# Optimization experiments

Measured on AMD Instinct MI355X. Metric: run time of the kernel, lower is better.

The kernel has to match this reference:

```python
import jax, jax.numpy as jnp
import numpy as np

NUM_HEADS = 8
ROPE_MIN_LOG = -12.0
ROPE_MAX_LOG = 0.0
EPS = 1e-6


def rms_norm(h, w):
    # per-head-dim RMSNorm in fp32 (Qwen3 style), no shift applied in forward
    dt = h.dtype
    h32 = h.astype(jnp.float32)
    var = jnp.mean(h32 * h32, axis=-1, keepdims=True)
    return (w * (h32 * jax.lax.rsqrt(var + EPS))).astype(dt)


def setup_inputs() -> dict:
    key = jax.random.key(0)
    k1, k2, k3 = jax.random.split(key, 3)
    B, H, W, C = 1, 256, 256, 512
    x = jax.random.normal(k1, (B, H, W, C), dtype=jnp.float32)
    w_qkv = jax.random.normal(k2, (3 * C, C), dtype=jnp.float32) * 0.02
    hd = C // NUM_HEADS
    q_norm_w = jnp.ones((hd,), dtype=jnp.float32)
    k_norm_w = jnp.ones((hd,), dtype=jnp.float32)
    w_proj = jax.random.normal(k3, (C, C), dtype=jnp.float32) * 0.02
    b_proj = jnp.zeros((C,), dtype=jnp.float32)
    return {"x": x, "w_qkv": w_qkv, "q_norm_w": q_norm_w, "k_norm_w": k_norm_w,
            "w_proj": w_proj, "b_proj": b_proj}


def reference(x, w_qkv, q_norm_w, k_norm_w, w_proj, b_proj):
    B, H, W, C = x.shape
    nh = NUM_HEADS
    hd = C // nh
    rope_dim = (hd // 2) * 2
    half = rope_dim // 2
    scale = hd ** -0.5

    # [B,H,W,C] -> [B*W, H, C]
    xr = jnp.transpose(x, (0, 2, 1, 3)).reshape(B * W, H, C)
    qkv = jnp.einsum('bhc,dc->bhd', xr, w_qkv)                # [BW, H, 3C]
    qkv = qkv.reshape(B * W, H, 3, nh, hd)
    qkv = jnp.transpose(qkv, (2, 0, 3, 1, 4))                 # [3, BW, nh, H, hd]
    q, k, v = qkv[0], qkv[1], qkv[2]

    q = rms_norm(q, q_norm_w)
    k = rms_norm(k, k_norm_w)

    # segmented-exponential RoPE along trace axis H (default normalized pos)
    pos = jnp.linspace(0.0, 1.0, H, dtype=jnp.float32)        # [H]
    freqs = jnp.exp(jnp.linspace(ROPE_MIN_LOG, ROPE_MAX_LOG, half, dtype=jnp.float32))
    ang = pos[:, None] * freqs[None, :] * jnp.float32(H)      # [H, half]
    cos = jnp.cos(ang)
    sin = jnp.sin(ang)

    def rope(t):
        rot = t[..., :rope_dim].reshape(B * W, nh, H, half, 2)
        te, to = rot[..., 0], rot[..., 1]
        e2 = te * cos - to * sin
        o2 = te * sin + to * cos
        rot2 = jnp.stack([e2, o2], axis=-1).reshape(B * W, nh, H, rope_dim)
        return jnp.concatenate([rot2, t[..., rope_dim:]], axis=-1)

    q = rope(q)
    k = rope(k)

    # SDPA (non-causal, no dropout)
    scores = jnp.einsum('bnqd,bnkd->bnqk', q, k) * scale      # [BW, nh, H, H]
    attn = jax.nn.softmax(scores, axis=-1)
    o = jnp.einsum('bnqk,bnkd->bnqd', attn, v)                # [BW, nh, H, hd]

    o = jnp.transpose(o, (0, 2, 1, 3)).reshape(B * W, H, C)
    out = jnp.einsum('bhc,dc->bhd', o, w_proj) + b_proj
    out = out.reshape(B, W, H, C)
    return jnp.transpose(out, (0, 2, 1, 3))                   # [B, H, W, C]
```

## Files before the change

### kernel.cpp

```cpp
#include <hip/hip_runtime.h>
#include <hip/hip_bf16.h>
#include <cstdint>
#include <cstddef>

#define SEQ 256
#define WDIM 256
#define CDIM 512
#define NHEAD 8
#define HD 64
#define NTOK (SEQ*WDIM)
#define NTT 8

typedef __attribute__((ext_vector_type(8))) short bf16x8;
typedef __attribute__((ext_vector_type(4))) float f32x4;

static __device__ __forceinline__ unsigned short f2bf(float f) {
  __hip_bfloat16 h = __float2bfloat16(f);
  return *reinterpret_cast<unsigned short*>(&h);
}

__global__ void k_convert(const float* __restrict__ x,
                          const float* __restrict__ wqkv,
                          const float* __restrict__ wproj,
                          unsigned short* __restrict__ xb,
                          unsigned short* __restrict__ wqb,
                          unsigned short* __restrict__ wpb) {
  const int NX = NTOK*CDIM/4, NQ = 3*CDIM*CDIM/4, NP = CDIM*CDIM/4;
  const int total = NX + NQ + NP;
  for (int i = blockIdx.x*blockDim.x + threadIdx.x; i < total; i += gridDim.x*blockDim.x) {
    const float4* s; unsigned short* d; int j;
    if (i < NX)           { s = (const float4*)x;     d = xb;  j = i; }
    else if (i < NX+NQ)   { s = (const float4*)wqkv;  d = wqb; j = i-NX; }
    else                  { s = (const float4*)wproj; d = wpb; j = i-NX-NQ; }
    float4 f = s[j];
    ushort4 o;
    o.x = f2bf(f.x); o.y = f2bf(f.y); o.z = f2bf(f.z); o.w = f2bf(f.w);
    ((ushort4*)d)[j] = o;
  }
}

__global__ void k_rope(float2* __restrict__ tab) {
  int i = blockIdx.x*blockDim.x + threadIdx.x;
  if (i >= SEQ*32) return;
  int h = i >> 5, j = i & 31;
  float freq = expf(-12.0f + 12.0f*(float)j/31.0f);
  float ang = ((float)h/255.0f) * freq * 256.0f;
  tab[i] = make_float2(cosf(ang), sinf(ang));
}


#define STAGE_G(tau_, part_)                                                              \
  if ((tau_) < NTT) {                                                                     \
    const int buf_ = (tau_) & 1;                                                          \
    const int ab_ = (part_) >> 1, hh_ = (part_) & 1;                                      \
    const unsigned short* src_ = ab_ ? B : A;                                             \
    const int row0_ = (ab_ ? rowB0 : rowA0) + hh_*128;                                    \
    _Pragma("unroll")                                                                     \
    for (int c_ = 0; c_ < 2; ++c_) {                                                      \
      int G_ = wid*128 + c_*64 + lane;                                                    \
      int r_ = G_ >> 3, g_ = G_ & 7;                                                      \
      int gsw_ = g_ ^ (r_ & 7);                                                           \
      __builtin_amdgcn_global_load_lds(                                                   \
        (const __attribute__((address_space(1))) unsigned int*)                           \
          ((const char*)src_ + (size_t)(row0_ + r_)*1024 + (size_t)(tau_)*128 + gsw_*16), \
        (__attribute__((address_space(3))) unsigned int*)                                 \
          ((char*)&L[buf_][ab_][hh_][0] + G_*16),                                         \
        16, 0, 0);                                                                        \
    }                                                                                     \
  }

#define LDA_(dst, m_, kk_)                                                                 \
  { int r_ = (m_)*16 + li;                                                                 \
    dst = *(const bf16x8*)((const char*)&L[buf][0][wr][0] + r_*128 + (((((kk_)*4)+lg) ^ (r_ & 7))<<4)); }
#define LDB_(dst, n_, kk_)                                                                 \
  { int r_ = (wc & 1)*64 + (n_)*16 + li;                                                   \
    dst = *(const bf16x8*)((const char*)&L[buf][1][wc>>1][0] + r_*128 + (((((kk_)*4)+lg) ^ (r_ & 7))<<4)); }

#define PH_SYNC                                            \
  __builtin_amdgcn_s_barrier();                            \
  asm volatile("s_waitcnt lgkmcnt(0)" ::: "memory");       \
  __builtin_amdgcn_sched_barrier(0);

#define MFMA16(afr, bfr, mo)                                                               \
  __builtin_amdgcn_s_setprio(1);                                                          \
  _Pragma("unroll")                                                                        \
  for (int m = 0; m < 4; ++m)                                                              \
    _Pragma("unroll")                                                                      \
    for (int n = 0; n < 4; ++n)                                                            \
      acc[m+(mo)][n] = __builtin_amdgcn_mfma_f32_16x16x32_bf16(afr[m], bfr[n], acc[m+(mo)][n], 0, 0, 0); \
  __builtin_amdgcn_s_setprio(0);

__device__ __forceinline__ void gemm256(const unsigned short* __restrict__ A,
                                        const unsigned short* __restrict__ B,
                                        int rowA0, int rowB0,
                                        unsigned short (&L)[2][2][2][128*64],
                                        f32x4 (&acc)[8][4]) {
  const int tid = threadIdx.x;
  const int lane = tid & 63, wid = tid >> 6;
  const int wr = wid >> 2, wc = wid & 3;
  const int li = lane & 15, lg = lane >> 4;

  STAGE_G(0,0) STAGE_G(0,1) STAGE_G(0,2) STAGE_G(0,3) STAGE_G(1,0) STAGE_G(1,1)
  asm volatile("s_waitcnt vmcnt(4)" ::: "memory");
  __builtin_amdgcn_s_barrier();

  #pragma unroll 1
  for (int tau = 0; tau < NTT; ++tau) {
    const int buf = tau & 1;
    bf16x8 a0[4], a1[4], aL0[4], aL1[4], bb0[4], bb1[4];
    #pragma unroll
    for (int m = 0; m < 4; ++m) LDA_(a0[m], m, 0);
    #pragma unroll
    for (int n = 0; n < 4; ++n) LDB_(bb0[n], n, 0);
    STAGE_G(tau+1, 2)
    PH_SYNC
    MFMA16(a0, bb0, 0)
    __builtin_amdgcn_s_barrier();
    #pragma unroll
    for (int m = 0; m < 4; ++m) LDA_(a1[m], m+4, 0);
    #pragma unroll
    for (int m = 0; m < 4; ++m) LDA_(aL0[m], m, 1);
    STAGE_G(tau+1, 3)
    PH_SYNC
    MFMA16(a1, bb0, 4)
    __builtin_amdgcn_s_barrier();
    #pragma unroll
    for (int m = 0; m < 4; ++m) LDA_(aL1[m], m+4, 1);
    #pragma unroll
    for (int n = 0; n < 4; ++n) LDB_(bb1[n], n, 1);
    PH_SYNC
    MFMA16(aL0, bb1, 0)
    __builtin_amdgcn_s_barrier();
    STAGE_G(tau+2, 0)
    STAGE_G(tau+2, 1)
    __builtin_amdgcn_sched_barrier(0);
    MFMA16(aL1, bb1, 4)
    if (tau < NTT-2) { asm volatile("s_waitcnt vmcnt(4)" ::: "memory"); }
    else             { asm volatile("s_waitcnt vmcnt(0)" ::: "memory"); }
    __builtin_amdgcn_s_barrier();
  }
}

__launch_bounds__(512)
__global__ void k_qkv(const unsigned short* __restrict__ A,
                      const unsigned short* __restrict__ B,
                      const float* __restrict__ qnw, const float* __restrict__ knw,
                      const float2* __restrict__ rope,
                      unsigned short* __restrict__ Qw,
                      unsigned short* __restrict__ Kw,
                      unsigned short* __restrict__ Vw) {
  __shared__ __align__(16) unsigned short L[2][2][2][128*64];
  int wg = (blockIdx.x & 7)*192 + (blockIdx.x >> 3);
  int bn = wg % 6, bm = wg / 6;
  f32x4 acc[8][4] = {};
  gemm256(A, B, bm*256, bn*256, L, acc);

  const int lane = threadIdx.x & 63, wid = threadIdx.x >> 6;
  const int wr = wid >> 2, wc = wid & 3;
  const int li = lane & 15, lg = lane >> 4;
  int d0 = bn*256 + wc*64;
  int third = d0 >> 9;
  int nhh = (d0 >> 6) & 7;
  int t0 = bm*256 + wr*128;
  int hpos = bm;

  if (third == 2) {
    #pragma unroll
    for (int m = 0; m < 8; ++m)
      #pragma unroll
      for (int n = 0; n < 4; ++n)
        #pragma unroll
        for (int r = 0; r < 4; ++r) {
          int t = t0 + m*16 + lg*4 + r;
          int wI = t & 255;
          int e = n*16 + li;
          Vw[((size_t)(wI*8 + nhh)*256 + hpos)*64 + e] = f2bf(acc[m][n][r]);
        }
  } else {
    const float* nw = (third == 0) ? qnw : knw;
    unsigned short* dst = (third == 0) ? Qw : Kw;
    const float qsc = (third == 0) ? 0.125f : 1.0f;
    float nwv[4]; float2 cs[4];
    #pragma unroll
    for (int n = 0; n < 4; ++n) {
      int e = n*16 + li;
      nwv[n] = nw[e];
      cs[n] = rope[hpos*32 + (e >> 1)];
    }
    bool odd = (li & 1) != 0;
    #pragma unroll
    for (int m = 0; m < 8; ++m) {
      float rsg[4];
      #pragma unroll
      for (int r = 0; r < 4; ++r) {
        float p = 0.f;
        #pragma unroll
        for (int n = 0; n < 4; ++n) p += acc[m][n][r]*acc[m][n][r];
        #pragma unroll
        for (int d = 1; d < 16; d <<= 1) p += __shfl_xor(p, d, 64);
        rsg[r] = rsqrtf(p*(1.0f/64.0f) + 1e-6f);
      }
      #pragma unroll
      for (int n = 0; n < 4; ++n)
        #pragma unroll
        for (int r = 0; r < 4; ++r) {
          float v = acc[m][n][r] * rsg[r] * nwv[n];
          float pr = __shfl_xor(v, 1, 64);
          float res = odd ? (pr*cs[n].y + v*cs[n].x) : (v*cs[n].x - pr*cs[n].y);
          res *= qsc;
          int t = t0 + m*16 + lg*4 + r;
          int wI = t & 255;
          int e = n*16 + li;
          dst[((size_t)(wI*8 + nhh)*256 + hpos)*64 + e] = f2bf(res);
        }
    }
  }
}

__launch_bounds__(256, 2)
__global__ void k_attn(const unsigned short* __restrict__ Q,
                       const unsigned short* __restrict__ K,
                       const unsigned short* __restrict__ V,
                       unsigned short* __restrict__ O) {
  __shared__ __align__(16) unsigned short P_lds[4][64*64];
  __shared__ __align__(16) unsigned short VT_lds[64*72];
  __shared__ __align__(16) unsigned short V_stage[64*64];
  int b = blockIdx.x;
  const unsigned short* Qb = Q + (size_t)b*SEQ*HD;
  const unsigned short* Kb = K + (size_t)b*SEQ*HD;
  const unsigned short* Vb = V + (size_t)b*SEQ*HD;
  const int lane = threadIdx.x & 63, wid = threadIdx.x >> 6;
  const int li = lane & 15, lg = lane >> 4;
  const int q0 = wid*64;
  char* Pw = (char*)&P_lds[wid][0];

#define STAGE_V(c_)                                                                       \
  { _Pragma("unroll")                                                                     \
    for (int r_ = 0; r_ < 2; ++r_) {                                                      \
      int D_ = wid*128 + r_*64 + lane;                                                    \
      int kl_ = D_ >> 3, g_ = (D_ & 7) ^ (kl_ & 7);                                       \
      __builtin_amdgcn_global_load_lds(                                                   \
        (const __attribute__((address_space(1))) unsigned int*)                           \
          (Vb + (size_t)((c_)*64 + kl_)*64 + g_*8),                                       \
        (__attribute__((address_space(3))) unsigned int*)((char*)V_stage + D_*16),        \
        16, 0, 0);                                                                        \
    } }

  STAGE_V(0)

  bf16x8 qf[4][2];
  #pragma unroll
  for (int n = 0; n < 4; ++n)
    #pragma unroll
    for (int kk = 0; kk < 2; ++kk)
      qf[n][kk] = *(const bf16x8*)(Qb + (q0 + n*16 + li)*64 + kk*32 + lg*8);

  f32x4 oa[4][4] = {};
  float mrun[4], lrun[4];
  #pragma unroll
  for (int n = 0; n < 4; ++n) { mrun[n] = -1e30f; lrun[n] = 0.0f; }

  #pragma unroll 1
  for (int kb = 0; kb < 4; ++kb) {
    int key0 = kb*64;
    f32x4 s[4][4] = {};
    #pragma unroll
    for (int kk = 0; kk < 2; ++kk) {
      bf16x8 kf[4];
      #pragma unroll
      for (int m = 0; m < 4; ++m)
        kf[m] = *(const bf16x8*)(Kb + (key0 + m*16 + li)*64 + kk*32 + lg*8);
      __builtin_amdgcn_s_setprio(1);
      #pragma unroll
      for (int m = 0; m < 4; ++m)
        #pragma unroll
        for (int n = 0; n < 4; ++n)
          s[m][n] = __builtin_amdgcn_mfma_f32_16x16x32_bf16(kf[m], qf[n][kk], s[m][n], 0, 0, 0);
      __builtin_amdgcn_s_setprio(0);
    }
    float mx[4], al[4];
    #pragma unroll
    for (int n = 0; n < 4; ++n) {
      float v = -1e30f;
      #pragma unroll
      for (int m = 0; m < 4; ++m)
        #pragma unroll
        for (int r = 0; r < 4; ++r) v = fmaxf(v, s[m][n][r]);
      v = fmaxf(v, __shfl_xor(v, 16, 64));
      v = fmaxf(v, __shfl_xor(v, 32, 64));
      float mn = fmaxf(mrun[n], v);
      al[n] = __expf(mrun[n] - mn);
      mrun[n] = mn;
      mx[n] = mn;
    }
    float rs[4] = {0.f,0.f,0.f,0.f};
    #pragma unroll
    for (int m = 0; m < 4; ++m)
      #pragma unroll
      for (int n = 0; n < 4; ++n) {
        f32x4 sv = s[m][n];
        #pragma unroll
        for (int r = 0; r < 4; ++r) {
          float p = __expf(sv[r] - mx[n]);
          sv[r] = p; rs[n] += p;
        }
        unsigned lo = (unsigned)f2bf(sv[0]) | ((unsigned)f2bf(sv[1]) << 16);
        unsigned hi = (unsigned)f2bf(sv[2]) | ((unsigned)f2bf(sv[3]) << 16);
        uint2 pk; pk.x = lo; pk.y = hi;
        int q = n*16 + li;
        int off = (q*128 + (m*16 + lg*4)*2) ^ ((li & 7) << 4);
        *(uint2*)(Pw + off) = pk;
      }
    #pragma unroll
    for (int n = 0; n < 4; ++n) {
      rs[n] += __shfl_xor(rs[n], 16, 64);
      rs[n] += __shfl_xor(rs[n], 32, 64);
      lrun[n] = lrun[n]*al[n] + rs[n];
    }
    #pragma unroll
    for (int mp = 0; mp < 4; ++mp)
      #pragma unroll
      for (int r = 0; r < 4; ++r) {
        float a = __shfl(al[mp], lg*4 + r, 64);
        #pragma unroll
        for (int np = 0; np < 4; ++np) oa[mp][np][r] *= a;
      }
    asm volatile("s_waitcnt vmcnt(0)" ::: "memory");
    __builtin_amdgcn_s_barrier();
    #pragma unroll
    for (int gi = 0; gi < 2; ++gi) {
      int g = wid + gi*4;
      bf16x8 row = *(const bf16x8*)&V_stage[(lane*8 + (g ^ (lane & 7)))*8];
      #pragma unroll
      for (int j = 0; j < 8; ++j)
        VT_lds[(g*8 + j)*72 + lane] = (unsigned short)row[j];
    }
    __builtin_amdgcn_s_barrier();
    if (kb < 3) STAGE_V(kb+1)
    #pragma unroll
    for (int kk = 0; kk < 2; ++kk) {
      bf16x8 pf[4], vf[4];
      #pragma unroll
      for (int mp = 0; mp < 4; ++mp) {
        int q = mp*16 + li;
        int off = (q*128 + (kk*32 + lg*8)*2) ^ ((li & 7) << 4);
        pf[mp] = *(const bf16x8*)(Pw + off);
      }
      #pragma unroll
      for (int np = 0; np < 4; ++np)
        vf[np] = *(const bf16x8*)&VT_lds[(np*16 + li)*72 + kk*32 + lg*8];
      __builtin_amdgcn_s_setprio(1);
      #pragma unroll
      for (int mp = 0; mp < 4; ++mp)
        #pragma unroll
        for (int np = 0; np < 4; ++np)
          oa[mp][np] = __builtin_amdgcn_mfma_f32_16x16x32_bf16(pf[mp], vf[np], oa[mp][np], 0, 0, 0);
      __builtin_amdgcn_s_setprio(0);
    }
  }
  int wseq = b >> 3, whead = b & 7;
  #pragma unroll
  for (int mp = 0; mp < 4; ++mp)
    #pragma unroll
    for (int r = 0; r < 4; ++r) {
      float linv = 1.0f / __shfl(lrun[mp], lg*4 + r, 64);
      #pragma unroll
      for (int np = 0; np < 4; ++np) {
        int q = q0 + mp*16 + lg*4 + r;
        int e = np*16 + li;
        O[((size_t)q*WDIM + wseq)*CDIM + whead*HD + e] = f2bf(oa[mp][np][r] * linv);
      }
    }
}

__launch_bounds__(512)
__global__ void k_proj(const unsigned short* __restrict__ A,
                       const unsigned short* __restrict__ B,
                       const float* __restrict__ bias,
                       float* __restrict__ out) {
  __shared__ __align__(16) unsigned short L[2][2][2][128*64];
  int wg = (blockIdx.x & 7)*64 + (blockIdx.x >> 3);
  int bn = wg & 1, bm = wg >> 1;
  f32x4 acc[8][4] = {};
  gemm256(A, B, bm*256, bn*256, L, acc);

  const int lane = threadIdx.x & 63, wid = threadIdx.x >> 6;
  const int wr = wid >> 2, wc = wid & 3;
  const int li = lane & 15, lg = lane >> 4;
  int d0 = bn*256 + wc*64;
  int t0 = bm*256 + wr*128;
  float bi[4];
  #pragma unroll
  for (int n = 0; n < 4; ++n) bi[n] = bias[d0 + n*16 + li];
  #pragma unroll
  for (int m = 0; m < 8; ++m)
    #pragma unroll
    for (int n = 0; n < 4; ++n)
      #pragma unroll
      for (int r = 0; r < 4; ++r)
        out[(size_t)(t0 + m*16 + lg*4 + r)*CDIM + d0 + n*16 + li] = acc[m][n][r] + bi[n];
}

extern "C" void kernel_launch(void* const* d_in, const int* in_sizes, int n_in,
                              void* d_out, int out_size, void* d_ws, size_t ws_size,
                              hipStream_t stream) {
  (void)in_sizes; (void)n_in; (void)out_size; (void)ws_size;
  const float* x     = (const float*)d_in[0];
  const float* wqkv  = (const float*)d_in[1];
  const float* qnw   = (const float*)d_in[2];
  const float* knw   = (const float*)d_in[3];
  const float* wproj = (const float*)d_in[4];
  const float* bproj = (const float*)d_in[5];
  float* out = (float*)d_out;
  char* ws = (char*)d_ws;

  const size_t SZ_X = (size_t)NTOK*CDIM*2;
  unsigned short* xb  = (unsigned short*)(ws);
  unsigned short* wqb = (unsigned short*)(ws + SZ_X);
  unsigned short* wpb = (unsigned short*)(ws + SZ_X + 1572864);
  float2*         rp  = (float2*)       (ws + SZ_X + 1572864 + 524288);
  unsigned short* Qw  = (unsigned short*)(ws + SZ_X + 1572864 + 524288 + 65536);
  unsigned short* Kw  = (unsigned short*)((char*)Qw + SZ_X);
  unsigned short* Vw  = (unsigned short*)((char*)Kw + SZ_X);
  unsigned short* Ow  = xb;

  k_convert<<<dim3(2048), dim3(256), 0, stream>>>(x, wqkv, wproj, xb, wqb, wpb);
  k_rope   <<<dim3(32),   dim3(256), 0, stream>>>(rp);
  k_qkv    <<<dim3(1536), dim3(512), 0, stream>>>(xb, wqb, qnw, knw, rp, Qw, Kw, Vw);
  k_attn   <<<dim3(2048), dim3(256), 0, stream>>>(Qw, Kw, Vw, Ow);
  k_proj   <<<dim3(512),  dim3(512), 0, stream>>>(Ow, wpb, bproj, out);
}
```

Baseline: 322.7 us.

## Fuse fp32-to-bf16 conversion of x into QKV GEMM A-operand loading

Drops the separate conversion pass over the 64K×512 activation tensor. The QKV GEMM now reads fp32 x straight into registers, converts it to bf16 and writes it into swizzled LDS, while B still uses direct global-to-LDS loads. This saves a full write and re-read of a 64 MB bf16 copy and one kernel launch. In exchange the GEMM reads fp32 A tiles at twice the byte volume, and each tile is re-read once per column block (six times). The register staging adds VGPR pressure and extra waitcnt/barrier points in the pipelined loop.

```diff
diff --git a/kernel.cpp b/kernel.cpp
--- a/kernel.cpp
+++ b/kernel.cpp
@@ -13,30 +13,24 @@
 
 typedef __attribute__((ext_vector_type(8))) short bf16x8;
 typedef __attribute__((ext_vector_type(4))) float f32x4;
+typedef __attribute__((ext_vector_type(8))) unsigned short u16x8;
 
 static __device__ __forceinline__ unsigned short f2bf(float f) {
   __hip_bfloat16 h = __float2bfloat16(f);
   return *reinterpret_cast<unsigned short*>(&h);
 }
 
-__global__ void k_convert(const float* __restrict__ x,
-                          const float* __restrict__ wqkv,
-                          const float* __restrict__ wproj,
-                          unsigned short* __restrict__ xb,
-                          unsigned short* __restrict__ wqb,
-                          unsigned short* __restrict__ wpb) {
-  const int NX = NTOK*CDIM/4, NQ = 3*CDIM*CDIM/4, NP = CDIM*CDIM/4;
-  const int total = NX + NQ + NP;
-  for (int i = blockIdx.x*blockDim.x + threadIdx.x; i < total; i += gridDim.x*blockDim.x) {
-    const float4* s; unsigned short* d; int j;
-    if (i < NX)           { s = (const float4*)x;     d = xb;  j = i; }
-    else if (i < NX+NQ)   { s = (const float4*)wqkv;  d = wqb; j = i-NX; }
-    else                  { s = (const float4*)wproj; d = wpb; j = i-NX-NQ; }
-    float4 f = s[j];
-    ushort4 o;
-    o.x = f2bf(f.x); o.y = f2bf(f.y); o.z = f2bf(f.z); o.w = f2bf(f.w);
-    ((ushort4*)d)[j] = o;
-  }
+__global__ void k_convw(const float* __restrict__ wqkv, const float* __restrict__ wproj,
+                        unsigned short* __restrict__ wqb, unsigned short* __restrict__ wpb) {
+  const int NQ = 3*CDIM*CDIM/4;
+  int i = blockIdx.x*blockDim.x + threadIdx.x;
+  const float4* s; unsigned short* d; int j;
+  if (i < NQ) { s = (const float4*)wqkv;  d = wqb; j = i; }
+  else        { s = (const float4*)wproj; d = wpb; j = i - NQ; }
+  float4 f = s[j];
+  ushort4 o;
+  o.x = f2bf(f.x); o.y = f2bf(f.y); o.z = f2bf(f.z); o.w = f2bf(f.w);
+  ((ushort4*)d)[j] = o;
 }
 
 __global__ void k_rope(float2* __restrict__ tab) {
@@ -48,6 +42,27 @@
   tab[i] = make_float2(cosf(ang), sinf(ang));
 }
 
+
+#define LDA_(dst, m_, kk_)                                                                 \
+  { int r_ = (m_)*16 + li;                                                                 \
+    dst = *(const bf16x8*)((const char*)&L[buf][0][wr][0] + r_*128 + (((((kk_)*4)+lg) ^ (r_ & 7))<<4)); }
+#define LDB_(dst, n_, kk_)                                                                 \
+  { int r_ = (wc & 1)*64 + (n_)*16 + li;                                                   \
+    dst = *(const bf16x8*)((const char*)&L[buf][1][wc>>1][0] + r_*128 + (((((kk_)*4)+lg) ^ (r_ & 7))<<4)); }
+
+#define PH_SYNC                                            \
+  __builtin_amdgcn_s_barrier();                            \
+  asm volatile("s_waitcnt lgkmcnt(0)" ::: "memory");       \
+  __builtin_amdgcn_sched_barrier(0);
+
+#define MFMA16(afr, bfr, mo)                                                               \
+  __builtin_amdgcn_s_setprio(1);                                                          \
+  _Pragma("unroll")                                                                        \
+  for (int m = 0; m < 4; ++m)                                                              \
+    _Pragma("unroll")                                                                      \
+    for (int n = 0; n < 4; ++n)                                                            \
+      acc[m+(mo)][n] = __builtin_amdgcn_mfma_f32_16x16x32_bf16(afr[m], bfr[n], acc[m+(mo)][n], 0, 0, 0); \
+  __builtin_amdgcn_s_setprio(0);
 
 #define STAGE_G(tau_, part_)                                                              \
   if ((tau_) < NTT) {                                                                     \
@@ -69,27 +84,6 @@
     }                                                                                     \
   }
 
-#define LDA_(dst, m_, kk_)                                                                 \
-  { int r_ = (m_)*16 + li;                                                                 \
-    dst = *(const bf16x8*)((const char*)&L[buf][0][wr][0] + r_*128 + (((((kk_)*4)+lg) ^ (r_ & 7))<<4)); }
-#define LDB_(dst, n_, kk_)                                                                 \
-  { int r_ = (wc & 1)*64 + (n_)*16 + li;                                                   \
-    dst = *(const bf16x8*)((const char*)&L[buf][1][wc>>1][0] + r_*128 + (((((kk_)*4)+lg) ^ (r_ & 7))<<4)); }
-
-#define PH_SYNC                                            \
-  __builtin_amdgcn_s_barrier();                            \
-  asm volatile("s_waitcnt lgkmcnt(0)" ::: "memory");       \
-  __builtin_amdgcn_sched_barrier(0);
-
-#define MFMA16(afr, bfr, mo)                                                               \
-  __builtin_amdgcn_s_setprio(1);                                                          \
-  _Pragma("unroll")                                                                        \
-  for (int m = 0; m < 4; ++m)                                                              \
-    _Pragma("unroll")                                                                      \
-    for (int n = 0; n < 4; ++n)                                                            \
-      acc[m+(mo)][n] = __builtin_amdgcn_mfma_f32_16x16x32_bf16(afr[m], bfr[n], acc[m+(mo)][n], 0, 0, 0); \
-  __builtin_amdgcn_s_setprio(0);
-
 __device__ __forceinline__ void gemm256(const unsigned short* __restrict__ A,
                                         const unsigned short* __restrict__ B,
                                         int rowA0, int rowB0,
@@ -141,8 +135,109 @@
   }
 }
 
+
+#define STAGE_B(tau_, hh_)                                                                \
+  if ((tau_) < NTT) {                                                                     \
+    const int buf_ = (tau_) & 1;                                                          \
+    _Pragma("unroll")                                                                     \
+    for (int c_ = 0; c_ < 2; ++c_) {                                                      \
+      int G_ = wid*128 + c_*64 + lane;                                                    \
+      int r_ = G_ >> 3, g_ = G_ & 7;                                                      \
+      int gsw_ = g_ ^ (r_ & 7);                                                           \
+      __builtin_amdgcn_global_load_lds(                                                   \
+        (const __attribute__((address_space(1))) unsigned int*)                           \
+          ((const char*)B + (size_t)(rowB0 + (hh_)*128 + r_)*1024 + (size_t)(tau_)*128 + gsw_*16), \
+        (__attribute__((address_space(3))) unsigned int*)                                 \
+          ((char*)&L[buf_][1][hh_][0] + G_*16),                                           \
+        16, 0, 0);                                                                        \
+    }                                                                                     \
+  }
+
+#define ALOAD_H(tau_, h_)                                                                 \
+  if ((tau_) < NTT) {                                                                     \
+    _Pragma("unroll")                                                                     \
+    for (int j_ = 0; j_ < 4; ++j_)                                                        \
+      areg[h_][j_] = *(const float4*)((const char*)A +                                    \
+        (size_t)(rowA0 + (h_)*128 + arow)*2048 + (size_t)(tau_)*256 + acb + j_*16);       \
+  }
+
+#define AWRITE_H(tau_, h_)                                                                \
+  if ((tau_) < NTT) {                                                                     \
+    const int buf_ = (tau_) & 1;                                                          \
+    _Pragma("unroll")                                                                     \
+    for (int gi_ = 0; gi_ < 2; ++gi_) {                                                   \
+      float4 f0 = areg[h_][gi_*2], f1 = areg[h_][gi_*2+1];                                \
+      u16x8 pk_;                                                                          \
+      pk_[0]=f2bf(f0.x); pk_[1]=f2bf(f0.y); pk_[2]=f2bf(f0.z); pk_[3]=f2bf(f0.w);         \
+      pk_[4]=f2bf(f1.x); pk_[5]=f2bf(f1.y); pk_[6]=f2bf(f1.z); pk_[7]=f2bf(f1.w);         \
+      int g_ = (acb >> 5) + gi_;                                                          \
+      *(u16x8*)((char*)&L[buf_][0][h_][0] + arow*128 + ((g_ ^ (arow & 7))<<4)) = pk_;     \
+    }                                                                                     \
+  }
+
+__device__ __forceinline__ void gemm256_f32(const float* __restrict__ A,
+                                            const unsigned short* __restrict__ B,
+                                            int rowA0, int rowB0,
+                                            unsigned short (&L)[2][2][2][128*64],
+                                            f32x4 (&acc)[8][4]) {
+  const int tid = threadIdx.x;
+  const int lane = tid & 63, wid = tid >> 6;
+  const int wr = wid >> 2, wc = wid & 3;
+  const int li = lane & 15, lg = lane >> 4;
+  const int arow = tid >> 2, acb = (tid & 3)*64;
+  float4 areg[2][4];
+
+  STAGE_B(0, 0) STAGE_B(0, 1)
+  ALOAD_H(0, 0) ALOAD_H(0, 1)
+  asm volatile("s_waitcnt vmcnt(0)" ::: "memory");
+  AWRITE_H(0, 0) AWRITE_H(0, 1)
+  asm volatile("s_waitcnt lgkmcnt(0)" ::: "memory");
+  __builtin_amdgcn_s_barrier();
+
+  #pragma unroll 1
+  for (int tau = 0; tau < NTT; ++tau) {
+    const int buf = tau & 1;
+    bf16x8 a0[4], a1[4], aL0[4], aL1[4], bb0[4], bb1[4];
+    #pragma unroll
+    for (int m = 0; m < 4; ++m) LDA_(a0[m], m, 0);
+    #pragma unroll
+    for (int n = 0; n < 4; ++n) LDB_(bb0[n], n, 0);
+    STAGE_B(tau+1, 0)
+    __builtin_amdgcn_sched_barrier(0);
+    ALOAD_H(tau+1, 0)
+    PH_SYNC
+    MFMA16(a0, bb0, 0)
+    __builtin_amdgcn_s_barrier();
+    #pragma unroll
+    for (int m = 0; m < 4; ++m) LDA_(a1[m], m+4, 0);
+    STAGE_B(tau+1, 1)
+    __builtin_amdgcn_sched_barrier(0);
+    ALOAD_H(tau+1, 1)
+    PH_SYNC
+    MFMA16(a1, bb0, 4)
+    __builtin_amdgcn_s_barrier();
+    #pragma unroll
+    for (int m = 0; m < 4; ++m) LDA_(aL0[m], m, 1);
+    #pragma unroll
+    for (int m = 0; m < 4; ++m) LDA_(aL1[m], m+4, 1);
+    #pragma unroll
+    for (int n = 0; n < 4; ++n) LDB_(bb1[n], n, 1);
+    asm volatile("s_waitcnt vmcnt(6)" ::: "memory");
+    AWRITE_H(tau+1, 0)
+    PH_SYNC
+    MFMA16(aL0, bb1, 0)
+    __builtin_amdgcn_s_barrier();
+    asm volatile("s_waitcnt vmcnt(0)" ::: "memory");
+    AWRITE_H(tau+1, 1)
+    __builtin_amdgcn_sched_barrier(0);
+    MFMA16(aL1, bb1, 4)
+    asm volatile("s_waitcnt lgkmcnt(0)" ::: "memory");
+    __builtin_amdgcn_s_barrier();
+  }
+}
+
 __launch_bounds__(512)
-__global__ void k_qkv(const unsigned short* __restrict__ A,
+__global__ void k_qkv(const float* __restrict__ A,
                       const unsigned short* __restrict__ B,
                       const float* __restrict__ qnw, const float* __restrict__ knw,
                       const float2* __restrict__ rope,
@@ -153,7 +248,7 @@
   int wg = (blockIdx.x & 7)*192 + (blockIdx.x >> 3);
   int bn = wg % 6, bm = wg / 6;
   f32x4 acc[8][4] = {};
-  gemm256(A, B, bm*256, bn*256, L, acc);
+  gemm256_f32(A, B, bm*256, bn*256, L, acc);
 
   const int lane = threadIdx.x & 63, wid = threadIdx.x >> 6;
   const int wr = wid >> 2, wc = wid & 3;
@@ -415,18 +510,17 @@
   char* ws = (char*)d_ws;
 
   const size_t SZ_X = (size_t)NTOK*CDIM*2;
-  unsigned short* xb  = (unsigned short*)(ws);
-  unsigned short* wqb = (unsigned short*)(ws + SZ_X);
-  unsigned short* wpb = (unsigned short*)(ws + SZ_X + 1572864);
-  float2*         rp  = (float2*)       (ws + SZ_X + 1572864 + 524288);
-  unsigned short* Qw  = (unsigned short*)(ws + SZ_X + 1572864 + 524288 + 65536);
+  unsigned short* wqb = (unsigned short*)(ws);
+  unsigned short* wpb = (unsigned short*)(ws + 1572864);
+  float2*         rp  = (float2*)       (ws + 1572864 + 524288);
+  unsigned short* Qw  = (unsigned short*)(ws + 1572864 + 524288 + 65536);
   unsigned short* Kw  = (unsigned short*)((char*)Qw + SZ_X);
   unsigned short* Vw  = (unsigned short*)((char*)Kw + SZ_X);
-  unsigned short* Ow  = xb;
-
-  k_convert<<<dim3(2048), dim3(256), 0, stream>>>(x, wqkv, wproj, xb, wqb, wpb);
+  unsigned short* Ow  = (unsigned short*)((char*)Vw + SZ_X);
+
+  k_convw  <<<dim3(1024), dim3(256), 0, stream>>>(wqkv, wproj, wqb, wpb);
   k_rope   <<<dim3(32),   dim3(256), 0, stream>>>(rp);
-  k_qkv    <<<dim3(1536), dim3(512), 0, stream>>>(xb, wqb, qnw, knw, rp, Qw, Kw, Vw);
+  k_qkv    <<<dim3(1536), dim3(512), 0, stream>>>(x, wqb, qnw, knw, rp, Qw, Kw, Vw);
   k_attn   <<<dim3(2048), dim3(256), 0, stream>>>(Qw, Kw, Vw, Ow);
   k_proj   <<<dim3(512),  dim3(512), 0, stream>>>(Ow, wpb, bproj, out);
 }
```

New measurement: 376.5 us. 1.17x slower.

## Prefetch V into registers and skip online-softmax rescale when max grows little

Applied to the files above, without the earlier changes.

V tiles are now prefetched straight into registers with plain global loads instead of async global-to-LDS staging, which removes the V_stage buffer and the vmcnt wait. Each wave also skips the running-max update and the rescaling of the output accumulator unless some row's max grows by more than 8, using a lazy-rescale threshold. This cuts exp and shuffle work and frees LDS, which may help occupancy. The cost is extra vector registers for vrow, and exponentials taken against a stale max can reach up to e^8, which still fits in fp32 and bf16.

```diff
diff --git a/kernel.cpp b/kernel.cpp
--- a/kernel.cpp
+++ b/kernel.cpp
@@ -224,7 +224,6 @@
                        unsigned short* __restrict__ O) {
   __shared__ __align__(16) unsigned short P_lds[4][64*64];
   __shared__ __align__(16) unsigned short VT_lds[64*72];
-  __shared__ __align__(16) unsigned short V_stage[64*64];
   int b = blockIdx.x;
   const unsigned short* Qb = Q + (size_t)b*SEQ*HD;
   const unsigned short* Kb = K + (size_t)b*SEQ*HD;
@@ -234,19 +233,10 @@
   const int q0 = wid*64;
   char* Pw = (char*)&P_lds[wid][0];
 
-#define STAGE_V(c_)                                                                       \
-  { _Pragma("unroll")                                                                     \
-    for (int r_ = 0; r_ < 2; ++r_) {                                                      \
-      int D_ = wid*128 + r_*64 + lane;                                                    \
-      int kl_ = D_ >> 3, g_ = (D_ & 7) ^ (kl_ & 7);                                       \
-      __builtin_amdgcn_global_load_lds(                                                   \
-        (const __attribute__((address_space(1))) unsigned int*)                           \
-          (Vb + (size_t)((c_)*64 + kl_)*64 + g_*8),                                       \
-        (__attribute__((address_space(3))) unsigned int*)((char*)V_stage + D_*16),        \
-        16, 0, 0);                                                                        \
-    } }
-
-  STAGE_V(0)
+  bf16x8 vrow[2];
+  #pragma unroll
+  for (int gi = 0; gi < 2; ++gi)
+    vrow[gi] = *(const bf16x8*)(Vb + (size_t)lane*64 + (wid + gi*4)*8);
 
   bf16x8 qf[4][2];
   #pragma unroll
@@ -278,7 +268,7 @@
           s[m][n] = __builtin_amdgcn_mfma_f32_16x16x32_bf16(kf[m], qf[n][kk], s[m][n], 0, 0, 0);
       __builtin_amdgcn_s_setprio(0);
     }
-    float mx[4], al[4];
+    float vmx[4];
     #pragma unroll
     for (int n = 0; n < 4; ++n) {
       float v = -1e30f;
@@ -288,10 +278,32 @@
         for (int r = 0; r < 4; ++r) v = fmaxf(v, s[m][n][r]);
       v = fmaxf(v, __shfl_xor(v, 16, 64));
       v = fmaxf(v, __shfl_xor(v, 32, 64));
-      float mn = fmaxf(mrun[n], v);
-      al[n] = __expf(mrun[n] - mn);
-      mrun[n] = mn;
-      mx[n] = mn;
+      vmx[n] = v;
+    }
+    float dmax = -1e30f;
+    #pragma unroll
+    for (int n = 0; n < 4; ++n) dmax = fmaxf(dmax, vmx[n] - mrun[n]);
+    float mx[4];
+    if (!__all(dmax <= 8.0f)) {
+      float al[4];
+      #pragma unroll
+      for (int n = 0; n < 4; ++n) {
+        float mn = fmaxf(mrun[n], vmx[n]);
+        al[n] = __expf(mrun[n] - mn);
+        mrun[n] = mn; mx[n] = mn;
+        lrun[n] *= al[n];
+      }
+      #pragma unroll
+      for (int mp = 0; mp < 4; ++mp)
+        #pragma unroll
+        for (int r = 0; r < 4; ++r) {
+          float a = __shfl(al[mp], lg*4 + r, 64);
+          #pragma unroll
+          for (int np = 0; np < 4; ++np) oa[mp][np][r] *= a;
+        }
+    } else {
+      #pragma unroll
+      for (int n = 0; n < 4; ++n) mx[n] = mrun[n];
     }
     float rs[4] = {0.f,0.f,0.f,0.f};
     #pragma unroll
@@ -315,28 +327,23 @@
     for (int n = 0; n < 4; ++n) {
       rs[n] += __shfl_xor(rs[n], 16, 64);
       rs[n] += __shfl_xor(rs[n], 32, 64);
-      lrun[n] = lrun[n]*al[n] + rs[n];
-    }
-    #pragma unroll
-    for (int mp = 0; mp < 4; ++mp)
-      #pragma unroll
-      for (int r = 0; r < 4; ++r) {
-        float a = __shfl(al[mp], lg*4 + r, 64);
-        #pragma unroll
-        for (int np = 0; np < 4; ++np) oa[mp][np][r] *= a;
-      }
-    asm volatile("s_waitcnt vmcnt(0)" ::: "memory");
+      lrun[n] += rs[n];
+    }
     __builtin_amdgcn_s_barrier();
     #pragma unroll
     for (int gi = 0; gi < 2; ++gi) {
       int g = wid + gi*4;
-      bf16x8 row = *(const bf16x8*)&V_stage[(lane*8 + (g ^ (lane & 7)))*8];
       #pragma unroll
       for (int j = 0; j < 8; ++j)
-        VT_lds[(g*8 + j)*72 + lane] = (unsigned short)row[j];
-    }
-    __builtin_amdgcn_s_barrier();
-    if (kb < 3) STAGE_V(kb+1)
+        VT_lds[(g*8 + j)*72 + lane] = (unsigned short)vrow[gi][j];
+    }
+    if (kb < 3) {
+      #pragma unroll
+      for (int gi = 0; gi < 2; ++gi)
+        vrow[gi] = *(const bf16x8*)(Vb + (size_t)((kb+1)*64 + lane)*64 + (wid + gi*4)*8);
+    }
+    asm volatile("s_waitcnt lgkmcnt(0)" ::: "memory");
+    __builtin_amdgcn_s_barrier();
     #pragma unroll
     for (int kk = 0; kk < 2; ++kk) {
       bf16x8 pf[4], vf[4];
```

After: 322.8 us. Within noise of the previous version (+0.0%).
